# Performance work log

Hardware: AMD Instinct MI355X
Metric: run time of the kernel (lower is better)

Reference implementation:

```python
import jax, jax.numpy as jnp
import numpy as np

D_MODEL = 1024
NUM_HEADS = 16
HEAD_DIM = D_MODEL // NUM_HEADS  # 64
# NOTE: the original module passes scale=attention_head_size, so scores are
# MULTIPLIED by head_dim (64), not divided by sqrt(head_dim). Faithful quirk.
SCALE = float(HEAD_DIM)


def setup_inputs() -> dict:
    key = jax.random.key(0)
    ks = jax.random.split(key, 6)
    bs, s, d = 2, 2048, D_MODEL
    q = jax.random.normal(ks[0], (bs, s, d), dtype=jnp.float32)
    k = jax.random.normal(ks[1], (bs, s, d), dtype=jnp.float32)
    v = jax.random.normal(ks[2], (bs, s, d), dtype=jnp.float32)
    # nn.Linear weights, shape (out, in); no bias (qkv_bias=False)
    init = 1.0 / np.sqrt(d)
    Wq = jax.random.uniform(ks[3], (d, d), jnp.float32, -init, init)
    Wk = jax.random.uniform(ks[4], (d, d), jnp.float32, -init, init)
    Wv = jax.random.uniform(ks[5], (d, d), jnp.float32, -init, init)
    return {"q": q, "k": k, "v": v, "Wq": Wq, "Wk": Wk, "Wv": Wv}


def _split_heads(x):
    bs, s, _ = x.shape
    return x.reshape(bs, s, NUM_HEADS, HEAD_DIM).transpose(0, 2, 1, 3)  # bhsd


def reference(q, k, v, Wq, Wk, Wv):
    bs, s, d = q.shape
    qh = _split_heads(q @ Wq.T)  # [b,h,s,hd]
    kh = _split_heads(k @ Wk.T)
    vh = _split_heads(v @ Wv.T)
    sims = jnp.einsum('bhqd,bhkd->bhqk', qh, kh) * SCALE
    attn = jax.nn.softmax(sims, axis=-1)
    out = jnp.einsum('bhqk,bhkd->bhqd', attn, vh)  # [b,h,s,hd]
    out = out.transpose(0, 2, 1, 3).reshape(bs, s, d)
    return out
```

## Files before the change

kernel.cpp:

```cpp
#include <hip/hip_runtime.h>


typedef _Float16 half4 __attribute__((ext_vector_type(4)));
typedef _Float16 half8 __attribute__((ext_vector_type(8)));
typedef float floatx4 __attribute__((ext_vector_type(4)));

#define MFMA_F16(a, b, c) __builtin_amdgcn_mfma_f32_16x16x32_f16((a), (b), (c), 0, 0, 0)

constexpr int SEQ = 2048;
constexpr int DM = 1024;
constexpr int NH = 16;
constexpr int HD = 64;
constexpr float QSCALE = 92.33248261689366f;

__device__ inline void split4(const float4 f, half4& h, half4& l) {
  h[0] = (_Float16)f.x; l[0] = (_Float16)(f.x - (float)h[0]);
  h[1] = (_Float16)f.y; l[1] = (_Float16)(f.y - (float)h[1]);
  h[2] = (_Float16)f.z; l[2] = (_Float16)(f.z - (float)h[2]);
  h[3] = (_Float16)f.w; l[3] = (_Float16)(f.w - (float)h[3]);
}

__global__ __launch_bounds__(256) void proj_kernel(
    const float* __restrict__ q, const float* __restrict__ k, const float* __restrict__ v,
    const float* __restrict__ Wq, const float* __restrict__ Wk, const float* __restrict__ Wv,
    _Float16* __restrict__ qh_hi, _Float16* __restrict__ qh_lo,
    _Float16* __restrict__ kh_hi, _Float16* __restrict__ kh_lo,
    _Float16* __restrict__ vh)
{
  const int z = blockIdx.z;
  const float* __restrict__ x = (z == 0) ? q : (z == 1) ? k : v;
  const float* __restrict__ W = (z == 0) ? Wq : (z == 1) ? Wk : Wv;

  __shared__ __align__(16) _Float16 As[2][128][40];
  __shared__ __align__(16) _Float16 Bs[2][128][40];

  const int tid = threadIdx.x;
  const int bm = blockIdx.x;
  const int bn = blockIdx.y;
  const int lane = tid & 63;
  const int l15 = lane & 15;
  const int quad = lane >> 4;
  const int w = tid >> 6;
  const int wm = w >> 1;
  const int wn = w & 1;

  floatx4 acc[4][4];
  #pragma unroll
  for (int mt = 0; mt < 4; mt++)
    #pragma unroll
    for (int nt = 0; nt < 4; nt++)
      acc[mt][nt] = (floatx4){0.f, 0.f, 0.f, 0.f};

  for (int kk = 0; kk < DM; kk += 32) {
    __syncthreads();
    #pragma unroll
    for (int i = 0; i < 4; i++) {
      int c = i * 256 + tid;
      int row = c >> 3;
      int col = (c & 7) * 4;
      float4 fa = *(const float4*)(x + (size_t)(bm * 128 + row) * DM + kk + col);
      float4 fb = *(const float4*)(W + (size_t)(bn * 128 + row) * DM + kk + col);
      half4 ah, al, bh_, bl_;
      split4(fa, ah, al);
      split4(fb, bh_, bl_);
      *(half4*)&As[0][row][col] = ah;
      *(half4*)&As[1][row][col] = al;
      *(half4*)&Bs[0][row][col] = bh_;
      *(half4*)&Bs[1][row][col] = bl_;
    }
    __syncthreads();

    half8 a_h[4], a_l[4], b_h[4], b_l[4];
    #pragma unroll
    for (int t = 0; t < 4; t++) {
      a_h[t] = *(const half8*)&As[0][wm * 64 + t * 16 + l15][quad * 8];
      a_l[t] = *(const half8*)&As[1][wm * 64 + t * 16 + l15][quad * 8];
      b_h[t] = *(const half8*)&Bs[0][wn * 64 + t * 16 + l15][quad * 8];
      b_l[t] = *(const half8*)&Bs[1][wn * 64 + t * 16 + l15][quad * 8];
    }
    if (z == 2) {
      #pragma unroll
      for (int mt = 0; mt < 4; mt++)
        #pragma unroll
        for (int nt = 0; nt < 4; nt++)
          acc[mt][nt] = MFMA_F16(a_h[mt], b_h[nt], acc[mt][nt]);
    } else {
      #pragma unroll
      for (int mt = 0; mt < 4; mt++)
        #pragma unroll
        for (int nt = 0; nt < 4; nt++) {
          floatx4 t0 = MFMA_F16(a_h[mt], b_h[nt], acc[mt][nt]);
          t0 = MFMA_F16(a_h[mt], b_l[nt], t0);
          acc[mt][nt] = MFMA_F16(a_l[mt], b_h[nt], t0);
        }
    }
  }

  const float scale = (z == 0) ? QSCALE : 1.0f;
  #pragma unroll
  for (int mt = 0; mt < 4; mt++)
    #pragma unroll
    for (int nt = 0; nt < 4; nt++)
      #pragma unroll
      for (int r = 0; r < 4; r++) {
        int gm = bm * 128 + wm * 64 + mt * 16 + quad * 4 + r;
        int gn = bn * 128 + wn * 64 + nt * 16 + l15;
        int b = gm >> 11, s = gm & 2047;
        int h = gn >> 6, hd = gn & 63;
        size_t idx = ((size_t)(b * NH + h) * SEQ + s) * HD + hd;
        float val = acc[mt][nt][r] * scale;
        if (z == 2) {
          vh[idx] = (_Float16)val;
        } else {
          _Float16 hi = (_Float16)val;
          _Float16 lo = (_Float16)(val - (float)hi);
          if (z == 0) { qh_hi[idx] = hi; qh_lo[idx] = lo; }
          else        { kh_hi[idx] = hi; kh_lo[idx] = lo; }
        }
      }
}

__global__ __launch_bounds__(256) void transpose_v(const _Float16* __restrict__ vh,
                                                   _Float16* __restrict__ vhT)
{
  __shared__ __align__(16) _Float16 T[128][72];
  const int bh = blockIdx.x;
  const int sc = blockIdx.y;
  const int tid = threadIdx.x;
  const _Float16* src = vh + ((size_t)bh * SEQ + sc * 128) * HD;
  #pragma unroll
  for (int i = 0; i < 4; i++) {
    int c = i * 256 + tid;
    int row = c >> 3, off = (c & 7) * 8;
    *(half8*)&T[row][off] = *(const half8*)(src + (size_t)row * HD + off);
  }
  __syncthreads();
  _Float16* dst = vhT + (size_t)bh * HD * SEQ + sc * 128;
  #pragma unroll
  for (int i = 0; i < 4; i++) {
    int c = i * 256 + tid;
    int hd = c >> 4, off = (c & 15) * 8;
    half8 vv;
    #pragma unroll
    for (int j = 0; j < 8; j++) vv[j] = T[off + j][hd];
    *(half8*)(dst + (size_t)hd * SEQ + off) = vv;
  }
}

__global__ __launch_bounds__(256, 4) void flash_kernel(
    const _Float16* __restrict__ qh_hi, const _Float16* __restrict__ qh_lo,
    const _Float16* __restrict__ kh_hi, const _Float16* __restrict__ kh_lo,
    const _Float16* __restrict__ vhT, float* __restrict__ out)
{
  __shared__ __align__(16) _Float16 Kh[64][72];
  __shared__ __align__(16) _Float16 Kl[64][72];
  __shared__ __align__(16) _Float16 Vt[64][72];
  __shared__ __align__(16) _Float16 PT[4][64][18];

  const int bh = blockIdx.x;
  const int qb = blockIdx.y;
  const int tid = threadIdx.x;
  const int wq = tid >> 6;
  const int lane = tid & 63;
  const int l15 = lane & 15;
  const int quad = lane >> 4;

  const size_t bh_off = (size_t)bh * SEQ * HD;
  const int qrow0 = qb * 64 + wq * 16;

  half8 bq_h[2], bq_l[2];
  {
    const _Float16* qp_h = qh_hi + bh_off + (size_t)(qrow0 + l15) * HD;
    const _Float16* qp_l = qh_lo + bh_off + (size_t)(qrow0 + l15) * HD;
    #pragma unroll
    for (int kc = 0; kc < 2; kc++) {
      bq_h[kc] = *(const half8*)(qp_h + kc * 32 + quad * 8);
      bq_l[kc] = *(const half8*)(qp_l + kc * 32 + quad * 8);
    }
  }

  float mrow = -3.0e38f, lrow = 0.f;
  floatx4 Oacc[4];
  #pragma unroll
  for (int nd = 0; nd < 4; nd++) Oacc[nd] = (floatx4){0.f, 0.f, 0.f, 0.f};

  for (int kt = 0; kt < SEQ / 64; kt++) {
    const int kbase = kt * 64;
    __syncthreads();
    {
      const _Float16* sk_h = kh_hi + bh_off + (size_t)kbase * HD;
      const _Float16* sk_l = kh_lo + bh_off + (size_t)kbase * HD;
      const _Float16* sv   = vhT + (size_t)bh * HD * SEQ + kbase;
      #pragma unroll
      for (int i = 0; i < 2; i++) {
        int c = i * 256 + tid;
        int row = c >> 3, off = (c & 7) * 8;
        *(half8*)&Kh[row][off] = *(const half8*)(sk_h + row * HD + off);
        *(half8*)&Kl[row][off] = *(const half8*)(sk_l + row * HD + off);
        *(half8*)&Vt[row][off] = *(const half8*)(sv + (size_t)row * SEQ + off);
      }
    }
    __syncthreads();

    floatx4 sacc[4];
    #pragma unroll
    for (int nt = 0; nt < 4; nt++) {
      half8 ak0 = *(const half8*)&Kh[nt * 16 + l15][quad * 8];
      half8 ak1 = *(const half8*)&Kh[nt * 16 + l15][32 + quad * 8];
      half8 am0 = *(const half8*)&Kl[nt * 16 + l15][quad * 8];
      half8 am1 = *(const half8*)&Kl[nt * 16 + l15][32 + quad * 8];
      floatx4 s4 = (floatx4){0.f, 0.f, 0.f, 0.f};
      s4 = MFMA_F16(ak0, bq_h[0], s4);
      s4 = MFMA_F16(ak1, bq_h[1], s4);
      s4 = MFMA_F16(ak0, bq_l[0], s4);
      s4 = MFMA_F16(ak1, bq_l[1], s4);
      s4 = MFMA_F16(am0, bq_h[0], s4);
      s4 = MFMA_F16(am1, bq_h[1], s4);
      sacc[nt] = s4;
    }

    float rmax = sacc[0][0];
    #pragma unroll
    for (int nt = 0; nt < 4; nt++)
      #pragma unroll
      for (int r = 0; r < 4; r++) rmax = fmaxf(rmax, sacc[nt][r]);
    rmax = fmaxf(rmax, __shfl_xor(rmax, 16, 64));
    rmax = fmaxf(rmax, __shfl_xor(rmax, 32, 64));
    const float mnew = fmaxf(mrow, rmax);
    const float alpha = exp2f(mrow - mnew);
    mrow = mnew;

    float rsum = 0.f;
    #pragma unroll
    for (int nt = 0; nt < 4; nt++)
      #pragma unroll
      for (int r = 0; r < 4; r++) {
        float p = exp2f(sacc[nt][r] - mnew);
        rsum += p;
        PT[wq][nt * 16 + quad * 4 + r][l15] = (_Float16)p;
      }
    rsum += __shfl_xor(rsum, 16, 64);
    rsum += __shfl_xor(rsum, 32, 64);
    lrow = lrow * alpha + rsum;
    #pragma unroll
    for (int nd = 0; nd < 4; nd++) {
      Oacc[nd][0] *= alpha; Oacc[nd][1] *= alpha;
      Oacc[nd][2] *= alpha; Oacc[nd][3] *= alpha;
    }

    #pragma unroll
    for (int kc = 0; kc < 2; kc++) {
      half8 bp;
      #pragma unroll
      for (int j = 0; j < 8; j++)
        bp[j] = PT[wq][kc * 32 + quad * 8 + j][l15];
      #pragma unroll
      for (int nd = 0; nd < 4; nd++) {
        half8 av = *(const half8*)&Vt[nd * 16 + l15][kc * 32 + quad * 8];
        Oacc[nd] = MFMA_F16(av, bp, Oacc[nd]);
      }
    }
  }

  const int b = bh >> 4, h = bh & 15;
  const int s = qb * 64 + wq * 16 + l15;
  const float rinv = 1.0f / lrow;
  float* obase = out + (size_t)(b * SEQ + s) * DM + h * HD;
  #pragma unroll
  for (int nd = 0; nd < 4; nd++) {
    float4 vv;
    vv.x = Oacc[nd][0] * rinv;
    vv.y = Oacc[nd][1] * rinv;
    vv.z = Oacc[nd][2] * rinv;
    vv.w = Oacc[nd][3] * rinv;
    *(float4*)(obase + nd * 16 + quad * 4) = vv;
  }
}

extern "C" void kernel_launch(void* const* d_in, const int* in_sizes, int n_in,
                              void* d_out, int out_size, void* d_ws, size_t ws_size,
                              hipStream_t stream) {
  const float* q  = (const float*)d_in[0];
  const float* k  = (const float*)d_in[1];
  const float* v  = (const float*)d_in[2];
  const float* Wq = (const float*)d_in[3];
  const float* Wk = (const float*)d_in[4];
  const float* Wv = (const float*)d_in[5];
  float* out = (float*)d_out;

  const size_t SZ = (size_t)2 * NH * SEQ * HD;
  _Float16* ws    = (_Float16*)d_ws;
  _Float16* qh_hi = ws + 0 * SZ;
  _Float16* qh_lo = ws + 1 * SZ;
  _Float16* kh_hi = ws + 2 * SZ;
  _Float16* kh_lo = ws + 3 * SZ;
  _Float16* vh    = ws + 4 * SZ;
  _Float16* vhT   = ws + 5 * SZ;

  proj_kernel<<<dim3(32, 8, 3), 256, 0, stream>>>(q, k, v, Wq, Wk, Wv,
                                                  qh_hi, qh_lo, kh_hi, kh_lo, vh);
  transpose_v<<<dim3(32, 16), 256, 0, stream>>>(vh, vhT);
  flash_kernel<<<dim3(32, 32), 256, 0, stream>>>(qh_hi, qh_lo, kh_hi, kh_lo, vhT, out);
}
```

Measured before the change: 326.2 us.

## Make flash kernel single-wave, register-resident with direct global K/V loads

The flash attention kernel now runs one 64-lane wave per block. Each wave handles two 16-row query groups and loads K hi/lo and transposed V fragments straight from global memory into registers instead of staging them through shared memory. The probability tile goes from accumulator registers directly into MFMA operands, with no LDS round trip. This removes all shared memory and block barriers, but every wave now fetches K/V from global or L2 on its own, and register pressure is higher.

Result: slower. 438.8 us (+34.5%).

```diff
diff --git a/kernel.cpp b/kernel.cpp
--- a/kernel.cpp
+++ b/kernel.cpp
@@ -147,133 +147,141 @@
   }
 }
 
-__global__ __launch_bounds__(256, 4) void flash_kernel(
+__global__ __launch_bounds__(64, 2) void flash_kernel(
     const _Float16* __restrict__ qh_hi, const _Float16* __restrict__ qh_lo,
     const _Float16* __restrict__ kh_hi, const _Float16* __restrict__ kh_lo,
     const _Float16* __restrict__ vhT, float* __restrict__ out)
 {
-  __shared__ __align__(16) _Float16 Kh[64][72];
-  __shared__ __align__(16) _Float16 Kl[64][72];
-  __shared__ __align__(16) _Float16 Vt[64][72];
-  __shared__ __align__(16) _Float16 PT[4][64][18];
-
   const int bh = blockIdx.x;
   const int qb = blockIdx.y;
-  const int tid = threadIdx.x;
-  const int wq = tid >> 6;
-  const int lane = tid & 63;
+  const int lane = threadIdx.x;
   const int l15 = lane & 15;
   const int quad = lane >> 4;
 
   const size_t bh_off = (size_t)bh * SEQ * HD;
-  const int qrow0 = qb * 64 + wq * 16;
-
-  half8 bq_h[2], bq_l[2];
-  {
-    const _Float16* qp_h = qh_hi + bh_off + (size_t)(qrow0 + l15) * HD;
-    const _Float16* qp_l = qh_lo + bh_off + (size_t)(qrow0 + l15) * HD;
+  const _Float16* __restrict__ kh_p = kh_hi + bh_off;
+  const _Float16* __restrict__ kl_p = kh_lo + bh_off;
+  const _Float16* __restrict__ vt_p = vhT + (size_t)bh * HD * SEQ;
+  const int qrow0 = qb * 32;
+
+  half8 bqh[2][2], bql[2][2];
+  #pragma unroll
+  for (int g = 0; g < 2; g++) {
+    const _Float16* qp_h = qh_hi + bh_off + (size_t)(qrow0 + g * 16 + l15) * HD;
+    const _Float16* qp_l = qh_lo + bh_off + (size_t)(qrow0 + g * 16 + l15) * HD;
     #pragma unroll
     for (int kc = 0; kc < 2; kc++) {
-      bq_h[kc] = *(const half8*)(qp_h + kc * 32 + quad * 8);
-      bq_l[kc] = *(const half8*)(qp_l + kc * 32 + quad * 8);
-    }
-  }
-
-  float mrow = -3.0e38f, lrow = 0.f;
-  floatx4 Oacc[4];
-  #pragma unroll
-  for (int nd = 0; nd < 4; nd++) Oacc[nd] = (floatx4){0.f, 0.f, 0.f, 0.f};
+      bqh[g][kc] = *(const half8*)(qp_h + kc * 32 + quad * 8);
+      bql[g][kc] = *(const half8*)(qp_l + kc * 32 + quad * 8);
+    }
+  }
+
+  float m_[2] = {-3.0e38f, -3.0e38f};
+  float l_[2] = {0.f, 0.f};
+  floatx4 Oacc[2][4];
+  #pragma unroll
+  for (int g = 0; g < 2; g++)
+    #pragma unroll
+    for (int nd = 0; nd < 4; nd++) Oacc[g][nd] = (floatx4){0.f, 0.f, 0.f, 0.f};
 
   for (int kt = 0; kt < SEQ / 64; kt++) {
     const int kbase = kt * 64;
-    __syncthreads();
-    {
-      const _Float16* sk_h = kh_hi + bh_off + (size_t)kbase * HD;
-      const _Float16* sk_l = kh_lo + bh_off + (size_t)kbase * HD;
-      const _Float16* sv   = vhT + (size_t)bh * HD * SEQ + kbase;
-      #pragma unroll
-      for (int i = 0; i < 2; i++) {
-        int c = i * 256 + tid;
-        int row = c >> 3, off = (c & 7) * 8;
-        *(half8*)&Kh[row][off] = *(const half8*)(sk_h + row * HD + off);
-        *(half8*)&Kl[row][off] = *(const half8*)(sk_l + row * HD + off);
-        *(half8*)&Vt[row][off] = *(const half8*)(sv + (size_t)row * SEQ + off);
-      }
-    }
-    __syncthreads();
-
-    floatx4 sacc[4];
+
+    half8 akh[4][2], akl[4][2];
     #pragma unroll
     for (int nt = 0; nt < 4; nt++) {
-      half8 ak0 = *(const half8*)&Kh[nt * 16 + l15][quad * 8];
-      half8 ak1 = *(const half8*)&Kh[nt * 16 + l15][32 + quad * 8];
-      half8 am0 = *(const half8*)&Kl[nt * 16 + l15][quad * 8];
-      half8 am1 = *(const half8*)&Kl[nt * 16 + l15][32 + quad * 8];
-      floatx4 s4 = (floatx4){0.f, 0.f, 0.f, 0.f};
-      s4 = MFMA_F16(ak0, bq_h[0], s4);
-      s4 = MFMA_F16(ak1, bq_h[1], s4);
-      s4 = MFMA_F16(ak0, bq_l[0], s4);
-      s4 = MFMA_F16(ak1, bq_l[1], s4);
-      s4 = MFMA_F16(am0, bq_h[0], s4);
-      s4 = MFMA_F16(am1, bq_h[1], s4);
-      sacc[nt] = s4;
-    }
-
-    float rmax = sacc[0][0];
-    #pragma unroll
-    for (int nt = 0; nt < 4; nt++)
-      #pragma unroll
-      for (int r = 0; r < 4; r++) rmax = fmaxf(rmax, sacc[nt][r]);
-    rmax = fmaxf(rmax, __shfl_xor(rmax, 16, 64));
-    rmax = fmaxf(rmax, __shfl_xor(rmax, 32, 64));
-    const float mnew = fmaxf(mrow, rmax);
-    const float alpha = exp2f(mrow - mnew);
-    mrow = mnew;
-
-    float rsum = 0.f;
-    #pragma unroll
-    for (int nt = 0; nt < 4; nt++)
-      #pragma unroll
-      for (int r = 0; r < 4; r++) {
-        float p = exp2f(sacc[nt][r] - mnew);
-        rsum += p;
-        PT[wq][nt * 16 + quad * 4 + r][l15] = (_Float16)p;
-      }
-    rsum += __shfl_xor(rsum, 16, 64);
-    rsum += __shfl_xor(rsum, 32, 64);
-    lrow = lrow * alpha + rsum;
+      const _Float16* krh = kh_p + (size_t)(kbase + 16 * nt + l15) * HD + quad * 8;
+      const _Float16* krl = kl_p + (size_t)(kbase + 16 * nt + l15) * HD + quad * 8;
+      #pragma unroll
+      for (int kc = 0; kc < 2; kc++) {
+        akh[nt][kc] = *(const half8*)(krh + kc * 32);
+        akl[nt][kc] = *(const half8*)(krl + kc * 32);
+      }
+    }
+    half8 av[4][2];
     #pragma unroll
     for (int nd = 0; nd < 4; nd++) {
-      Oacc[nd][0] *= alpha; Oacc[nd][1] *= alpha;
-      Oacc[nd][2] *= alpha; Oacc[nd][3] *= alpha;
-    }
-
-    #pragma unroll
-    for (int kc = 0; kc < 2; kc++) {
-      half8 bp;
-      #pragma unroll
-      for (int j = 0; j < 8; j++)
-        bp[j] = PT[wq][kc * 32 + quad * 8 + j][l15];
+      const _Float16* vr = vt_p + (size_t)(nd * 16 + l15) * SEQ + kbase + quad * 4;
+      #pragma unroll
+      for (int kc = 0; kc < 2; kc++) {
+        half4 lo = *(const half4*)(vr + kc * 32);
+        half4 hi = *(const half4*)(vr + kc * 32 + 16);
+        #pragma unroll
+        for (int j = 0; j < 4; j++) { av[nd][kc][j] = lo[j]; av[nd][kc][j + 4] = hi[j]; }
+      }
+    }
+
+    #pragma unroll
+    for (int g = 0; g < 2; g++) {
+      floatx4 sacc[4];
+      #pragma unroll
+      for (int nt = 0; nt < 4; nt++) {
+        floatx4 s4 = (floatx4){0.f, 0.f, 0.f, 0.f};
+        s4 = MFMA_F16(akh[nt][0], bqh[g][0], s4);
+        s4 = MFMA_F16(akh[nt][1], bqh[g][1], s4);
+        s4 = MFMA_F16(akh[nt][0], bql[g][0], s4);
+        s4 = MFMA_F16(akh[nt][1], bql[g][1], s4);
+        s4 = MFMA_F16(akl[nt][0], bqh[g][0], s4);
+        s4 = MFMA_F16(akl[nt][1], bqh[g][1], s4);
+        sacc[nt] = s4;
+      }
+
+      float rmax = sacc[0][0];
+      #pragma unroll
+      for (int nt = 0; nt < 4; nt++)
+        #pragma unroll
+        for (int r = 0; r < 4; r++) rmax = fmaxf(rmax, sacc[nt][r]);
+      rmax = fmaxf(rmax, __shfl_xor(rmax, 16, 64));
+      rmax = fmaxf(rmax, __shfl_xor(rmax, 32, 64));
+      const float mnew = fmaxf(m_[g], rmax);
+      const float alpha = exp2f(m_[g] - mnew);
+      m_[g] = mnew;
+
+      float p[4][4];
+      float rsum = 0.f;
+      #pragma unroll
+      for (int nt = 0; nt < 4; nt++)
+        #pragma unroll
+        for (int r = 0; r < 4; r++) {
+          p[nt][r] = exp2f(sacc[nt][r] - mnew);
+          rsum += p[nt][r];
+        }
+      rsum += __shfl_xor(rsum, 16, 64);
+      rsum += __shfl_xor(rsum, 32, 64);
+      l_[g] = l_[g] * alpha + rsum;
+
+      half8 bp8[2];
+      #pragma unroll
+      for (int kc = 0; kc < 2; kc++)
+        #pragma unroll
+        for (int j = 0; j < 8; j++)
+          bp8[kc][j] = (_Float16)p[2 * kc + (j >> 2)][j & 3];
+
       #pragma unroll
       for (int nd = 0; nd < 4; nd++) {
-        half8 av = *(const half8*)&Vt[nd * 16 + l15][kc * 32 + quad * 8];
-        Oacc[nd] = MFMA_F16(av, bp, Oacc[nd]);
+        Oacc[g][nd][0] *= alpha; Oacc[g][nd][1] *= alpha;
+        Oacc[g][nd][2] *= alpha; Oacc[g][nd][3] *= alpha;
+        Oacc[g][nd] = MFMA_F16(av[nd][0], bp8[0], Oacc[g][nd]);
+        Oacc[g][nd] = MFMA_F16(av[nd][1], bp8[1], Oacc[g][nd]);
       }
     }
   }
 
   const int b = bh >> 4, h = bh & 15;
-  const int s = qb * 64 + wq * 16 + l15;
-  const float rinv = 1.0f / lrow;
-  float* obase = out + (size_t)(b * SEQ + s) * DM + h * HD;
-  #pragma unroll
-  for (int nd = 0; nd < 4; nd++) {
-    float4 vv;
-    vv.x = Oacc[nd][0] * rinv;
-    vv.y = Oacc[nd][1] * rinv;
-    vv.z = Oacc[nd][2] * rinv;
-    vv.w = Oacc[nd][3] * rinv;
-    *(float4*)(obase + nd * 16 + quad * 4) = vv;
+  #pragma unroll
+  for (int g = 0; g < 2; g++) {
+    const int s = qrow0 + g * 16 + l15;
+    const float rinv = 1.0f / l_[g];
+    float* obase = out + (size_t)(b * SEQ + s) * DM + h * HD;
+    #pragma unroll
+    for (int nd = 0; nd < 4; nd++) {
+      float4 vv;
+      vv.x = Oacc[g][nd][0] * rinv;
+      vv.y = Oacc[g][nd][1] * rinv;
+      vv.z = Oacc[g][nd][2] * rinv;
+      vv.w = Oacc[g][nd][3] * rinv;
+      *(float4*)(obase + nd * 16 + quad * 4) = vv;
+    }
   }
 }
 
@@ -300,5 +308,5 @@
   proj_kernel<<<dim3(32, 8, 3), 256, 0, stream>>>(q, k, v, Wq, Wk, Wv,
                                                   qh_hi, qh_lo, kh_hi, kh_lo, vh);
   transpose_v<<<dim3(32, 16), 256, 0, stream>>>(vh, vhT);
-  flash_kernel<<<dim3(32, 32), 256, 0, stream>>>(qh_hi, qh_lo, kh_hi, kh_lo, vhT, out);
-}
+  flash_kernel<<<dim3(32, 64), 64, 0, stream>>>(qh_hi, qh_lo, kh_hi, kh_lo, vhT, out);
+}
```
